# Performance work log

Hardware: AMD Instinct MI355X
Metric: run time of the kernel (lower is better)

Reference implementation:

```python
import jax, jax.numpy as jnp
import numpy as np

SIGMA = 0.05
N_IN, N_OUT, N_HID = 128, 128, 1024
BATCH, LENGTH = 128, 256


def setup_inputs() -> dict:
    key = jax.random.key(0)
    ks = jax.random.split(key, 8)
    input_signal = jax.random.normal(ks[0], (BATCH, LENGTH, N_IN), dtype=jnp.float32)
    hidden = jnp.zeros((BATCH, N_HID), dtype=jnp.float32)
    # learned params (torch nn.Linear stores weight as [out, in])
    W_in = jax.random.normal(ks[1], (N_HID, N_IN), dtype=jnp.float32) / np.sqrt(N_IN)
    W_hh = jax.random.normal(ks[2], (N_HID, N_HID), dtype=jnp.float32) / np.sqrt(N_HID)
    b_hh = jax.random.normal(ks[3], (N_HID,), dtype=jnp.float32) * 0.01
    W_out = jax.random.normal(ks[4], (N_OUT, N_HID), dtype=jnp.float32) / np.sqrt(N_HID)
    # frozen alpha vector (positive, used as sqrt(2/alpha))
    alpha_w = jax.random.uniform(ks[5], (N_HID,), dtype=jnp.float32, minval=5.0, maxval=25.0)
    # per-step noise, shared across batch (torch.randn(n_hid) each step)
    noise = jax.random.normal(ks[6], (LENGTH, N_HID), dtype=jnp.float32)
    return {"input_signal": input_signal, "hidden": hidden, "W_in": W_in,
            "W_hh": W_hh, "b_hh": b_hh, "W_out": W_out,
            "alpha_w": alpha_w, "noise": noise}


def reference(input_signal, hidden, W_in, W_hh, b_hh, W_out, alpha_w, noise):
    # input_signal: [B, T, n_in]; hidden: [B, n_hid]
    x_tbd = jnp.transpose(input_signal, (1, 0, 2))  # [T, B, n_in]
    noise_scale = jnp.sqrt(2.0 / alpha_w) * SIGMA    # [n_hid]

    def step(h, xs):
        x_t, n_t = xs
        pre = x_t @ W_in.T + h @ W_hh.T + b_hh + n_t * noise_scale
        h_new = jax.nn.relu(pre)
        y = h_new @ W_out.T
        return h_new, (h_new, y)

    h_final, (hs, ys) = jax.lax.scan(step, hidden, (x_tbd, noise))
    hidden_list = jnp.transpose(hs, (1, 0, 2))  # [B, T, n_hid]
    output_list = jnp.transpose(ys, (1, 0, 2))  # [B, T, n_out]
    return hidden_list, output_list, h_final
```

## Files before the change

kernel.cpp:

```cpp
#include <hip/hip_runtime.h>
#include <hip/hip_fp16.h>
#include <math.h>


typedef _Float16 half8 __attribute__((ext_vector_type(8)));
typedef float    f32x4 __attribute__((ext_vector_type(4)));
typedef unsigned short ushort8 __attribute__((ext_vector_type(8)));
typedef unsigned int u32x4 __attribute__((ext_vector_type(4)));
typedef unsigned long long u64;

#define SIGMA_F 0.05f

constexpr int T_  = 256;
constexpr int B_  = 128;
constexpr int NH  = 1024;
constexpr int NIN = 128;
constexpr int MB  = 16;

constexpr size_t OFF_XT  = 0;
constexpr size_t OFF_NB  = (size_t)T_*B_*NIN*2;
constexpr size_t OFF_WO  = OFF_NB + (size_t)T_*NH*4;
constexpr size_t OFF_HB  = OFF_WO + (size_t)NIN*NH*2;

__device__ __forceinline__ unsigned short f16bits(float v) {
    return __half_as_ushort(__float2half(v));
}
__device__ __forceinline__ u64 ald(const u64* p) {
    return __hip_atomic_load(p, __ATOMIC_RELAXED, __HIP_MEMORY_SCOPE_AGENT);
}
__device__ __forceinline__ void ast(unsigned int* p, unsigned int v) {
    __hip_atomic_store(p, v, __ATOMIC_RELAXED, __HIP_MEMORY_SCOPE_AGENT);
}

__device__ __forceinline__ void ld8_sc0(u32x4 r[8], const u64* p) {
    asm volatile(
        "global_load_dwordx4 %0, %8, off sc0\n\t"
        "global_load_dwordx4 %1, %8, off offset:256 sc0\n\t"
        "global_load_dwordx4 %2, %8, off offset:512 sc0\n\t"
        "global_load_dwordx4 %3, %8, off offset:768 sc0\n\t"
        "global_load_dwordx4 %4, %8, off offset:1024 sc0\n\t"
        "global_load_dwordx4 %5, %8, off offset:1280 sc0\n\t"
        "global_load_dwordx4 %6, %8, off offset:1536 sc0\n\t"
        "global_load_dwordx4 %7, %8, off offset:1792 sc0\n\t"
        "s_waitcnt vmcnt(0)"
        : "=&v"(r[0]), "=&v"(r[1]), "=&v"(r[2]), "=&v"(r[3]),
          "=&v"(r[4]), "=&v"(r[5]), "=&v"(r[6]), "=&v"(r[7])
        : "v"(p)
        : "memory");
}

__global__ void setup_kernel(const float* __restrict__ X,
                             const float* __restrict__ hidden,
                             const float* __restrict__ b_hh,
                             const float* __restrict__ W_out,
                             const float* __restrict__ alpha_w,
                             const float* __restrict__ noise,
                             unsigned short* __restrict__ Xt,
                             float* __restrict__ NB,
                             unsigned short* __restrict__ Wo,
                             unsigned int* __restrict__ Hb0,
                             unsigned int* __restrict__ Hb1)
{
    int idx = blockIdx.x * 256 + threadIdx.x;
    if (idx < B_ * T_ * NIN) {
        int d = idx & 127, rest = idx >> 7;
        int brow = rest & 127, t = rest >> 7;
        Xt[idx] = f16bits(X[((size_t)brow * T_ + t) * NIN + d]);
    }
    if (idx < T_ * NH) {
        int c = idx & (NH - 1);
        NB[idx] = b_hh[c] + noise[idx] * (sqrtf(2.0f / alpha_w[c]) * SIGMA_F);
    }
    if (idx < NIN * NH) Wo[idx] = f16bits(W_out[idx]);
    if (idx < B_ * NH / 2) {
        unsigned int lo = f16bits(hidden[idx * 2]);
        unsigned int hi = f16bits(hidden[idx * 2 + 1]);
        Hb0[idx] = (lo | (hi << 16)) & 0x7FFF7FFFu;
        Hb1[idx] = 0x80008000u;
    }
}

__global__ __launch_bounds__(256, 1) void rnn_step_kernel(
    const float* __restrict__ W_hh, const float* __restrict__ W_in,
    const unsigned short* __restrict__ Xt, const float* __restrict__ NB,
    unsigned int* __restrict__ Hb0, unsigned int* __restrict__ Hb1,
    float* __restrict__ hidden_list, float* __restrict__ h_final)
{
    __shared__ unsigned short wtile[64 * 960];
    __shared__ unsigned short htile[16 * 1024];

    const int tid = threadIdx.x;
    const int m = blockIdx.x & 7;
    const int n = blockIdx.x >> 3;

    for (int g = tid; g < 64 * 120; g += 256) {
        int row = g / 120, G = g - row * 120;
        const float* s = W_hh + (size_t)(n * 64 + row) * NH + G * 8;
        half8 h;
        #pragma unroll
        for (int j = 0; j < 8; ++j) h[j] = (_Float16)s[j];
        *(half8*)&wtile[row * 960 + ((G ^ (row & 7)) << 3)] = h;
    }

    const int wave = tid >> 6, lane = tid & 63;
    const int l15 = lane & 15, lk = lane >> 4;
    const int colW = wave * 16 + l15;
    const int gcol = n * 64 + colW;

    auto cvt8 = [](const float* s) {
        half8 h;
        #pragma unroll
        for (int j = 0; j < 8; ++j) h[j] = (_Float16)s[j];
        return h;
    };
    half8 bh30 = cvt8(W_hh + (size_t)gcol * NH + 960 + lk * 8);
    half8 bh31 = cvt8(W_hh + (size_t)gcol * NH + 992 + lk * 8);
    half8 bx[4];
    #pragma unroll
    for (int kx = 0; kx < 4; ++kx)
        bx[kx] = cvt8(W_in + (size_t)gcol * NIN + kx * 32 + lk * 8);
    __syncthreads();

    const int hrow = tid >> 4;
    const int part = tid & 15;

    auto xpart = [&](int t) -> f32x4 {
        f32x4 a = {0.f, 0.f, 0.f, 0.f};
        const int rowA = m * MB + l15;
        const ushort8* xp = (const ushort8*)(Xt + ((size_t)t * B_ + rowA) * NIN) + lk;
        #pragma unroll
        for (int kx = 0; kx < 4; ++kx) {
            half8 av = __builtin_bit_cast(half8, xp[kx * 4]);
            a = __builtin_amdgcn_mfma_f32_16x16x32_f16(av, bx[kx], a, 0, 0, 0);
        }
        return a;
    };

    f32x4 accx = xpart(0);

    for (int t = 0; t < T_; ++t) {
        const u64* hp = (const u64*)((t & 1) ? Hb1 : Hb0)
                        + (size_t)(m * MB + hrow) * 256 + part * 2;
        const unsigned int e32 = ((t >> 1) & 1) ? 0x80008000u : 0u;

        u32x4 r[8];
        int round = 0;
        for (;;) {
            if (round < 3) {
                ld8_sc0(r, hp);
            } else {
                #pragma unroll
                for (int j = 0; j < 8; ++j) {
                    u64 a = ald(hp + (size_t)j * 32);
                    u64 b = ald(hp + (size_t)j * 32 + 1);
                    r[j][0] = (unsigned int)a; r[j][1] = (unsigned int)(a >> 32);
                    r[j][2] = (unsigned int)b; r[j][3] = (unsigned int)(b >> 32);
                }
            }
            unsigned int red = 0;
            #pragma unroll
            for (int j = 0; j < 8; ++j) {
                #pragma unroll
                for (int k = 0; k < 4; ++k) red |= r[j][k] ^ e32;
            }
            if (!(red & 0x80008000u)) break;
            ++round;
            if (round >= 3) __builtin_amdgcn_s_sleep(1);
        }

        __syncthreads();

        #pragma unroll
        for (int j = 0; j < 8; ++j) {
            u32x4 w;
            #pragma unroll
            for (int k = 0; k < 4; ++k) w[k] = r[j][k] & 0x7FFF7FFFu;
            int G = j * 16 + part;
            *(half8*)&htile[hrow * 1024 + ((G ^ (hrow & 7)) << 3)] =
                __builtin_bit_cast(half8, w);
        }

        __syncthreads();

        f32x4 acc = accx;
        #pragma unroll
        for (int ki = 0; ki < 30; ++ki) {
            int G = 4 * ki + lk;
            half8 av = *(const half8*)&htile[l15 * 1024 + ((G ^ (l15 & 7)) << 3)];
            half8 bv = *(const half8*)&wtile[colW * 960 + ((G ^ (colW & 7)) << 3)];
            acc = __builtin_amdgcn_mfma_f32_16x16x32_f16(av, bv, acc, 0, 0, 0);
        }
        {
            int G = 120 + lk;
            half8 av = *(const half8*)&htile[l15 * 1024 + ((G ^ (l15 & 7)) << 3)];
            acc = __builtin_amdgcn_mfma_f32_16x16x32_f16(av, bh30, acc, 0, 0, 0);
            G = 124 + lk;
            av = *(const half8*)&htile[l15 * 1024 + ((G ^ (l15 & 7)) << 3)];
            acc = __builtin_amdgcn_mfma_f32_16x16x32_f16(av, bh31, acc, 0, 0, 0);
        }

        const float nb = NB[t * NH + gcol];
        float hv[4];
        #pragma unroll
        for (int r2 = 0; r2 < 4; ++r2) {
            float v = acc[r2] + nb;
            hv[r2] = v > 0.f ? v : 0.f;
        }

        if (t < T_ - 1) {
            unsigned int* hn = (t & 1) ? Hb0 : Hb1;
            const unsigned int tagb = (((t + 1) >> 1) & 1) ? 0x80008000u : 0u;
            #pragma unroll
            for (int r2 = 0; r2 < 4; ++r2) {
                float other = __shfl_xor(hv[r2], 1);
                if (!(lane & 1)) {
                    unsigned int val = (unsigned int)f16bits(hv[r2]) |
                                       ((unsigned int)f16bits(other) << 16) | tagb;
                    int brow = m * MB + lk * 4 + r2;
                    ast(&hn[(size_t)brow * 512 + (gcol >> 1)], val);
                }
            }
        }

        #pragma unroll
        for (int r2 = 0; r2 < 4; ++r2) {
            int brow = m * MB + lk * 4 + r2;
            hidden_list[((size_t)brow * T_ + t) * NH + gcol] = hv[r2];
        }
        if (t == T_ - 1) {
            #pragma unroll
            for (int r2 = 0; r2 < 4; ++r2) {
                int brow = m * MB + lk * 4 + r2;
                h_final[(size_t)brow * NH + gcol] = hv[r2];
            }
        } else {
            accx = xpart(t + 1);
        }
    }
}

__global__ __launch_bounds__(256, 4) void ygemm_kernel(
    const float* __restrict__ HL, const unsigned short* __restrict__ Wo,
    float* __restrict__ Y)
{
    const int tid = threadIdx.x;
    const int wave = tid >> 6, lane = tid & 63;
    const int l15 = lane & 15, lk = lane >> 4;
    const size_t rowbase = (size_t)blockIdx.x * 64;

    f32x4 acc[4][2] = {};

    #pragma unroll 2
    for (int ki = 0; ki < 32; ++ki) {
        const int k0 = ki * 32 + lk * 8;
        half8 bfr[2];
        #pragma unroll
        for (int nt = 0; nt < 2; ++nt) {
            int ncol = (wave * 2 + nt) * 16 + l15;
            ushort8 braw = *(const ushort8*)(Wo + ncol * NH + k0);
            bfr[nt] = __builtin_bit_cast(half8, braw);
        }
        #pragma unroll
        for (int mt = 0; mt < 4; ++mt) {
            size_t row = rowbase + mt * 16 + l15;
            const float4* ap = (const float4*)(HL + row * NH + k0);
            float4 a0 = ap[0];
            float4 a1 = ap[1];
            half8 a = { (_Float16)a0.x, (_Float16)a0.y, (_Float16)a0.z, (_Float16)a0.w,
                        (_Float16)a1.x, (_Float16)a1.y, (_Float16)a1.z, (_Float16)a1.w };
            #pragma unroll
            for (int nt = 0; nt < 2; ++nt)
                acc[mt][nt] = __builtin_amdgcn_mfma_f32_16x16x32_f16(a, bfr[nt], acc[mt][nt], 0, 0, 0);
        }
    }

    #pragma unroll
    for (int mt = 0; mt < 4; ++mt) {
        #pragma unroll
        for (int nt = 0; nt < 2; ++nt) {
            int ncol = (wave * 2 + nt) * 16 + l15;
            #pragma unroll
            for (int r = 0; r < 4; ++r) {
                size_t row = rowbase + mt * 16 + lk * 4 + r;
                Y[row * NIN + ncol] = acc[mt][nt][r];
            }
        }
    }
}

extern "C" void kernel_launch(void* const* d_in, const int* in_sizes, int n_in,
                              void* d_out, int out_size, void* d_ws, size_t ws_size,
                              hipStream_t stream)
{
    const float* X      = (const float*)d_in[0];
    const float* hidden = (const float*)d_in[1];
    const float* W_in   = (const float*)d_in[2];
    const float* W_hh   = (const float*)d_in[3];
    const float* b_hh   = (const float*)d_in[4];
    const float* W_out  = (const float*)d_in[5];
    const float* alpha  = (const float*)d_in[6];
    const float* noise  = (const float*)d_in[7];

    char* ws = (char*)d_ws;
    unsigned short* Xt = (unsigned short*)(ws + OFF_XT);
    float*          NB = (float*)(ws + OFF_NB);
    unsigned short* Wo = (unsigned short*)(ws + OFF_WO);
    unsigned int*  Hb0 = (unsigned int*)(ws + OFF_HB);
    unsigned int*  Hb1 = Hb0 + (size_t)B_ * NH / 2;

    float* hidden_list = (float*)d_out;
    float* output_list = hidden_list + (size_t)B_ * T_ * NH;
    float* h_final     = output_list + (size_t)B_ * T_ * NIN;

    setup_kernel<<<(B_ * T_ * NIN + 255) / 256, 256, 0, stream>>>(
        X, hidden, b_hh, W_out, alpha, noise, Xt, NB, Wo, Hb0, Hb1);

    rnn_step_kernel<<<128, 256, 0, stream>>>(
        W_hh, W_in, Xt, NB, Hb0, Hb1, hidden_list, h_final);

    ygemm_kernel<<<(B_ * T_) / 64, 256, 0, stream>>>(
        hidden_list, Wo, output_list);
}
```

Baseline: 823.2 us.

## Split recurrent GEMM across 256 blocks with intra-block K-split reduction

Each block now owns 32 hidden columns instead of 64, so the grid doubles to 256 blocks. Within a block, the four waves split the K dimension in halves and combine partial sums through a small shared tile. The whole W_hh slice now fits in LDS, so the register-held tail weights go away. This shortens the serial per-step MFMA chain but adds one more barrier per step and doubles the number of blocks in the cross-block spin-wait. Stores of hidden_list become nontemporal and the sc0 polling rounds are raised before the fallback.

```diff
diff --git a/kernel.cpp b/kernel.cpp
--- a/kernel.cpp
+++ b/kernel.cpp
@@ -5,7 +5,6 @@
 
 typedef _Float16 half8 __attribute__((ext_vector_type(8)));
 typedef float    f32x4 __attribute__((ext_vector_type(4)));
-typedef unsigned short ushort8 __attribute__((ext_vector_type(8)));
 typedef unsigned int u32x4 __attribute__((ext_vector_type(4)));
 typedef unsigned long long u64;
 
@@ -16,6 +15,7 @@
 constexpr int NH  = 1024;
 constexpr int NIN = 128;
 constexpr int MB  = 16;
+constexpr int NCB = 32;
 
 constexpr size_t OFF_XT  = 0;
 constexpr size_t OFF_NB  = (size_t)T_*B_*NIN*2;
@@ -86,26 +86,29 @@
     unsigned int* __restrict__ Hb0, unsigned int* __restrict__ Hb1,
     float* __restrict__ hidden_list, float* __restrict__ h_final)
 {
-    __shared__ unsigned short wtile[64 * 960];
+    __shared__ unsigned short wtile[NCB * 1024];
     __shared__ unsigned short htile[16 * 1024];
+    __shared__ f32x4 rtile[2][64];
 
     const int tid = threadIdx.x;
     const int m = blockIdx.x & 7;
     const int n = blockIdx.x >> 3;
 
-    for (int g = tid; g < 64 * 120; g += 256) {
-        int row = g / 120, G = g - row * 120;
-        const float* s = W_hh + (size_t)(n * 64 + row) * NH + G * 8;
+    for (int g = tid; g < NCB * 128; g += 256) {
+        int row = g >> 7, G = g & 127;
+        const float* s = W_hh + (size_t)(n * NCB + row) * NH + G * 8;
         half8 h;
         #pragma unroll
         for (int j = 0; j < 8; ++j) h[j] = (_Float16)s[j];
-        *(half8*)&wtile[row * 960 + ((G ^ (row & 7)) << 3)] = h;
+        *(half8*)&wtile[row * 1024 + ((G ^ (row & 7)) << 3)] = h;
     }
 
     const int wave = tid >> 6, lane = tid & 63;
+    const int c  = wave & 1;
+    const int kh = wave >> 1;
     const int l15 = lane & 15, lk = lane >> 4;
-    const int colW = wave * 16 + l15;
-    const int gcol = n * 64 + colW;
+    const int colW = c * 16 + l15;
+    const int gcol = n * NCB + colW;
 
     auto cvt8 = [](const float* s) {
         half8 h;
@@ -113,26 +116,24 @@
         for (int j = 0; j < 8; ++j) h[j] = (_Float16)s[j];
         return h;
     };
-    half8 bh30 = cvt8(W_hh + (size_t)gcol * NH + 960 + lk * 8);
-    half8 bh31 = cvt8(W_hh + (size_t)gcol * NH + 992 + lk * 8);
-    half8 bx[4];
+    half8 bx2[2];
     #pragma unroll
-    for (int kx = 0; kx < 4; ++kx)
-        bx[kx] = cvt8(W_in + (size_t)gcol * NIN + kx * 32 + lk * 8);
+    for (int j = 0; j < 2; ++j)
+        bx2[j] = cvt8(W_in + (size_t)gcol * NIN + (2 * kh + j) * 32 + lk * 8);
     __syncthreads();
 
     const int hrow = tid >> 4;
     const int part = tid & 15;
 
+    const int rowA = m * MB + l15;
+
     auto xpart = [&](int t) -> f32x4 {
         f32x4 a = {0.f, 0.f, 0.f, 0.f};
-        const int rowA = m * MB + l15;
-        const ushort8* xp = (const ushort8*)(Xt + ((size_t)t * B_ + rowA) * NIN) + lk;
-        #pragma unroll
-        for (int kx = 0; kx < 4; ++kx) {
-            half8 av = __builtin_bit_cast(half8, xp[kx * 4]);
-            a = __builtin_amdgcn_mfma_f32_16x16x32_f16(av, bx[kx], a, 0, 0, 0);
-        }
+        const half8* xp = (const half8*)(Xt + ((size_t)t * B_ + rowA) * NIN);
+        #pragma unroll
+        for (int j = 0; j < 2; ++j)
+            a = __builtin_amdgcn_mfma_f32_16x16x32_f16(
+                    xp[(2 * kh + j) * 4 + lk], bx2[j], a, 0, 0, 0);
         return a;
     };
 
@@ -144,28 +145,30 @@
         const unsigned int e32 = ((t >> 1) & 1) ? 0x80008000u : 0u;
 
         u32x4 r[8];
-        int round = 0;
-        for (;;) {
-            if (round < 3) {
-                ld8_sc0(r, hp);
-            } else {
+        {
+            int round = 0;
+            for (;;) {
+                if (round < 6) {
+                    ld8_sc0(r, hp);
+                } else {
+                    #pragma unroll
+                    for (int j = 0; j < 8; ++j) {
+                        u64 a = ald(hp + (size_t)j * 32);
+                        u64 b = ald(hp + (size_t)j * 32 + 1);
+                        r[j][0] = (unsigned int)a; r[j][1] = (unsigned int)(a >> 32);
+                        r[j][2] = (unsigned int)b; r[j][3] = (unsigned int)(b >> 32);
+                    }
+                }
+                unsigned int red = 0;
                 #pragma unroll
                 for (int j = 0; j < 8; ++j) {
-                    u64 a = ald(hp + (size_t)j * 32);
-                    u64 b = ald(hp + (size_t)j * 32 + 1);
-                    r[j][0] = (unsigned int)a; r[j][1] = (unsigned int)(a >> 32);
-                    r[j][2] = (unsigned int)b; r[j][3] = (unsigned int)(b >> 32);
+                    #pragma unroll
+                    for (int k = 0; k < 4; ++k) red |= r[j][k] ^ e32;
                 }
-            }
-            unsigned int red = 0;
-            #pragma unroll
-            for (int j = 0; j < 8; ++j) {
-                #pragma unroll
-                for (int k = 0; k < 4; ++k) red |= r[j][k] ^ e32;
-            }
-            if (!(red & 0x80008000u)) break;
-            ++round;
-            if (round >= 3) __builtin_amdgcn_s_sleep(1);
+                if (!(red & 0x80008000u)) break;
+                ++round;
+                if (round >= 3) __builtin_amdgcn_s_sleep(1);
+            }
         }
 
         __syncthreads();
@@ -184,58 +187,58 @@
 
         f32x4 acc = accx;
         #pragma unroll
-        for (int ki = 0; ki < 30; ++ki) {
+        for (int ki0 = 0; ki0 < 16; ++ki0) {
+            int ki = 16 * kh + ki0;
             int G = 4 * ki + lk;
             half8 av = *(const half8*)&htile[l15 * 1024 + ((G ^ (l15 & 7)) << 3)];
-            half8 bv = *(const half8*)&wtile[colW * 960 + ((G ^ (colW & 7)) << 3)];
+            half8 bv = *(const half8*)&wtile[colW * 1024 + ((G ^ (colW & 7)) << 3)];
             acc = __builtin_amdgcn_mfma_f32_16x16x32_f16(av, bv, acc, 0, 0, 0);
         }
-        {
-            int G = 120 + lk;
-            half8 av = *(const half8*)&htile[l15 * 1024 + ((G ^ (l15 & 7)) << 3)];
-            acc = __builtin_amdgcn_mfma_f32_16x16x32_f16(av, bh30, acc, 0, 0, 0);
-            G = 124 + lk;
-            av = *(const half8*)&htile[l15 * 1024 + ((G ^ (l15 & 7)) << 3)];
-            acc = __builtin_amdgcn_mfma_f32_16x16x32_f16(av, bh31, acc, 0, 0, 0);
-        }
-
-        const float nb = NB[t * NH + gcol];
-        float hv[4];
-        #pragma unroll
-        for (int r2 = 0; r2 < 4; ++r2) {
-            float v = acc[r2] + nb;
-            hv[r2] = v > 0.f ? v : 0.f;
-        }
-
-        if (t < T_ - 1) {
-            unsigned int* hn = (t & 1) ? Hb0 : Hb1;
-            const unsigned int tagb = (((t + 1) >> 1) & 1) ? 0x80008000u : 0u;
+
+        if (kh == 1) rtile[c][lane] = acc;
+        __syncthreads();
+
+        if (kh == 0) {
+            f32x4 o = rtile[c][lane];
+            const float nb = NB[t * NH + gcol];
+            float hv[4];
             #pragma unroll
             for (int r2 = 0; r2 < 4; ++r2) {
-                float other = __shfl_xor(hv[r2], 1);
-                if (!(lane & 1)) {
-                    unsigned int val = (unsigned int)f16bits(hv[r2]) |
-                                       ((unsigned int)f16bits(other) << 16) | tagb;
-                    int brow = m * MB + lk * 4 + r2;
-                    ast(&hn[(size_t)brow * 512 + (gcol >> 1)], val);
+                float v = acc[r2] + o[r2] + nb;
+                hv[r2] = v > 0.f ? v : 0.f;
+            }
+
+            if (t < T_ - 1) {
+                unsigned int* hn = (t & 1) ? Hb0 : Hb1;
+                const unsigned int tagb = (((t + 1) >> 1) & 1) ? 0x80008000u : 0u;
+                #pragma unroll
+                for (int r2 = 0; r2 < 4; ++r2) {
+                    float other = __shfl_xor(hv[r2], 1);
+                    if (!(lane & 1)) {
+                        unsigned int val = (unsigned int)f16bits(hv[r2]) |
+                                           ((unsigned int)f16bits(other) << 16) | tagb;
+                        int brow = m * MB + lk * 4 + r2;
+                        ast(&hn[(size_t)brow * 512 + (gcol >> 1)], val);
+                    }
                 }
             }
-        }
-
-        #pragma unroll
-        for (int r2 = 0; r2 < 4; ++r2) {
-            int brow = m * MB + lk * 4 + r2;
-            hidden_list[((size_t)brow * T_ + t) * NH + gcol] = hv[r2];
-        }
-        if (t == T_ - 1) {
+
             #pragma unroll
             for (int r2 = 0; r2 < 4; ++r2) {
                 int brow = m * MB + lk * 4 + r2;
-                h_final[(size_t)brow * NH + gcol] = hv[r2];
-            }
-        } else {
-            accx = xpart(t + 1);
-        }
+                __builtin_nontemporal_store(
+                    hv[r2], &hidden_list[((size_t)brow * T_ + t) * NH + gcol]);
+            }
+            if (t == T_ - 1) {
+                #pragma unroll
+                for (int r2 = 0; r2 < 4; ++r2) {
+                    int brow = m * MB + lk * 4 + r2;
+                    __builtin_nontemporal_store(
+                        hv[r2], &h_final[(size_t)brow * NH + gcol]);
+                }
+            }
+        }
+        if (t < T_ - 1) accx = xpart(t + 1);
     }
 }
 
@@ -243,6 +246,7 @@
     const float* __restrict__ HL, const unsigned short* __restrict__ Wo,
     float* __restrict__ Y)
 {
+    typedef unsigned short ushort8 __attribute__((ext_vector_type(8)));
     const int tid = threadIdx.x;
     const int wave = tid >> 6, lane = tid & 63;
     const int l15 = lane & 15, lk = lane >> 4;
@@ -315,7 +319,7 @@
     setup_kernel<<<(B_ * T_ * NIN + 255) / 256, 256, 0, stream>>>(
         X, hidden, b_hh, W_out, alpha, noise, Xt, NB, Wo, Hb0, Hb1);
 
-    rnn_step_kernel<<<128, 256, 0, stream>>>(
+    rnn_step_kernel<<<256, 256, 0, stream>>>(
         W_hh, W_in, Xt, NB, Hb0, Hb1, hidden_list, h_final);
 
     ygemm_kernel<<<(B_ * T_) / 64, 256, 0, stream>>>(
```

Result: slower. 1.766 ms (+114.5%).

## Add per-step per-row-group ready flags before polling tagged hidden state

Applied to the files above, without the earlier changes.

Adds a flag array with one flag per (timestep, batch group, producer wave). Each producer wave sets its flag after its hidden-state stores drain, and consumers poll a single dword per lane until all 64 flags are set before reading the tagged hidden buffers. The intent is to replace repeated polling of large 8x16B hidden loads with a cheap flag poll. The cost is an extra vmcnt wait plus a flag store on the producer side, and extra latency on the critical step-to-step path, while the old tag-check loop is still kept as a fallback.

```diff
diff --git a/kernel.cpp b/kernel.cpp
--- a/kernel.cpp
+++ b/kernel.cpp
@@ -5,7 +5,6 @@
 
 typedef _Float16 half8 __attribute__((ext_vector_type(8)));
 typedef float    f32x4 __attribute__((ext_vector_type(4)));
-typedef unsigned short ushort8 __attribute__((ext_vector_type(8)));
 typedef unsigned int u32x4 __attribute__((ext_vector_type(4)));
 typedef unsigned long long u64;
 
@@ -21,11 +20,15 @@
 constexpr size_t OFF_NB  = (size_t)T_*B_*NIN*2;
 constexpr size_t OFF_WO  = OFF_NB + (size_t)T_*NH*4;
 constexpr size_t OFF_HB  = OFF_WO + (size_t)NIN*NH*2;
+constexpr size_t OFF_FLG = OFF_HB + (size_t)2*B_*(NH/2)*4;
 
 __device__ __forceinline__ unsigned short f16bits(float v) {
     return __half_as_ushort(__float2half(v));
 }
 __device__ __forceinline__ u64 ald(const u64* p) {
+    return __hip_atomic_load(p, __ATOMIC_RELAXED, __HIP_MEMORY_SCOPE_AGENT);
+}
+__device__ __forceinline__ unsigned int ald32(const unsigned int* p) {
     return __hip_atomic_load(p, __ATOMIC_RELAXED, __HIP_MEMORY_SCOPE_AGENT);
 }
 __device__ __forceinline__ void ast(unsigned int* p, unsigned int v) {
@@ -49,6 +52,15 @@
         : "memory");
 }
 
+__device__ __forceinline__ unsigned int ld_flag_sc0(const unsigned int* p) {
+    unsigned int v;
+    asm volatile(
+        "global_load_dword %0, %1, off sc0\n\t"
+        "s_waitcnt vmcnt(0)"
+        : "=v"(v) : "v"(p) : "memory");
+    return v;
+}
+
 __global__ void setup_kernel(const float* __restrict__ X,
                              const float* __restrict__ hidden,
                              const float* __restrict__ b_hh,
@@ -59,7 +71,8 @@
                              float* __restrict__ NB,
                              unsigned short* __restrict__ Wo,
                              unsigned int* __restrict__ Hb0,
-                             unsigned int* __restrict__ Hb1)
+                             unsigned int* __restrict__ Hb1,
+                             unsigned int* __restrict__ FLG)
 {
     int idx = blockIdx.x * 256 + threadIdx.x;
     if (idx < B_ * T_ * NIN) {
@@ -78,12 +91,14 @@
         Hb0[idx] = (lo | (hi << 16)) & 0x7FFF7FFFu;
         Hb1[idx] = 0x80008000u;
     }
+    if (idx < T_ * 8 * 64) FLG[idx] = (idx < 8 * 64) ? 1u : 0u;
 }
 
 __global__ __launch_bounds__(256, 1) void rnn_step_kernel(
     const float* __restrict__ W_hh, const float* __restrict__ W_in,
     const unsigned short* __restrict__ Xt, const float* __restrict__ NB,
     unsigned int* __restrict__ Hb0, unsigned int* __restrict__ Hb1,
+    unsigned int* __restrict__ FLG,
     float* __restrict__ hidden_list, float* __restrict__ h_final)
 {
     __shared__ unsigned short wtile[64 * 960];
@@ -124,48 +139,60 @@
     const int hrow = tid >> 4;
     const int part = tid & 15;
 
+    const int rowA = m * MB + l15;
+
     auto xpart = [&](int t) -> f32x4 {
         f32x4 a = {0.f, 0.f, 0.f, 0.f};
-        const int rowA = m * MB + l15;
-        const ushort8* xp = (const ushort8*)(Xt + ((size_t)t * B_ + rowA) * NIN) + lk;
-        #pragma unroll
-        for (int kx = 0; kx < 4; ++kx) {
-            half8 av = __builtin_bit_cast(half8, xp[kx * 4]);
-            a = __builtin_amdgcn_mfma_f32_16x16x32_f16(av, bx[kx], a, 0, 0, 0);
-        }
+        const half8* xp = (const half8*)(Xt + ((size_t)t * B_ + rowA) * NIN) + lk;
+        #pragma unroll
+        for (int kx = 0; kx < 4; ++kx)
+            a = __builtin_amdgcn_mfma_f32_16x16x32_f16(xp[kx * 4], bx[kx], a, 0, 0, 0);
         return a;
     };
 
     f32x4 accx = xpart(0);
 
     for (int t = 0; t < T_; ++t) {
+        {
+            const unsigned int* fp = FLG + ((size_t)t * 8 + m) * 64 + lane;
+            int fr = 0;
+            for (;;) {
+                unsigned int fv = (fr < 6) ? ld_flag_sc0(fp) : ald32(fp);
+                if (__all(fv != 0u)) break;
+                ++fr;
+                if (fr >= 2) __builtin_amdgcn_s_sleep(2);
+            }
+        }
+
         const u64* hp = (const u64*)((t & 1) ? Hb1 : Hb0)
                         + (size_t)(m * MB + hrow) * 256 + part * 2;
         const unsigned int e32 = ((t >> 1) & 1) ? 0x80008000u : 0u;
 
         u32x4 r[8];
-        int round = 0;
-        for (;;) {
-            if (round < 3) {
-                ld8_sc0(r, hp);
-            } else {
+        {
+            int round = 0;
+            for (;;) {
+                if (round < 6) {
+                    ld8_sc0(r, hp);
+                } else {
+                    #pragma unroll
+                    for (int j = 0; j < 8; ++j) {
+                        u64 a = ald(hp + (size_t)j * 32);
+                        u64 b = ald(hp + (size_t)j * 32 + 1);
+                        r[j][0] = (unsigned int)a; r[j][1] = (unsigned int)(a >> 32);
+                        r[j][2] = (unsigned int)b; r[j][3] = (unsigned int)(b >> 32);
+                    }
+                }
+                unsigned int red = 0;
                 #pragma unroll
                 for (int j = 0; j < 8; ++j) {
-                    u64 a = ald(hp + (size_t)j * 32);
-                    u64 b = ald(hp + (size_t)j * 32 + 1);
-                    r[j][0] = (unsigned int)a; r[j][1] = (unsigned int)(a >> 32);
-                    r[j][2] = (unsigned int)b; r[j][3] = (unsigned int)(b >> 32);
+                    #pragma unroll
+                    for (int k = 0; k < 4; ++k) red |= r[j][k] ^ e32;
                 }
-            }
-            unsigned int red = 0;
-            #pragma unroll
-            for (int j = 0; j < 8; ++j) {
-                #pragma unroll
-                for (int k = 0; k < 4; ++k) red |= r[j][k] ^ e32;
-            }
-            if (!(red & 0x80008000u)) break;
-            ++round;
-            if (round >= 3) __builtin_amdgcn_s_sleep(1);
+                if (!(red & 0x80008000u)) break;
+                ++round;
+                if (round >= 3) __builtin_amdgcn_s_sleep(1);
+            }
         }
 
         __syncthreads();
@@ -220,6 +247,9 @@
                     ast(&hn[(size_t)brow * 512 + (gcol >> 1)], val);
                 }
             }
+            asm volatile("s_waitcnt vmcnt(0)" ::: "memory");
+            if (lane == 0)
+                ast(FLG + ((size_t)(t + 1) * 8 + m) * 64 + n * 4 + wave, 1u);
         }
 
         #pragma unroll
@@ -243,6 +273,7 @@
     const float* __restrict__ HL, const unsigned short* __restrict__ Wo,
     float* __restrict__ Y)
 {
+    typedef unsigned short ushort8 __attribute__((ext_vector_type(8)));
     const int tid = threadIdx.x;
     const int wave = tid >> 6, lane = tid & 63;
     const int l15 = lane & 15, lk = lane >> 4;
@@ -307,16 +338,17 @@
     unsigned short* Wo = (unsigned short*)(ws + OFF_WO);
     unsigned int*  Hb0 = (unsigned int*)(ws + OFF_HB);
     unsigned int*  Hb1 = Hb0 + (size_t)B_ * NH / 2;
+    unsigned int*  FLG = (unsigned int*)(ws + OFF_FLG);
 
     float* hidden_list = (float*)d_out;
     float* output_list = hidden_list + (size_t)B_ * T_ * NH;
     float* h_final     = output_list + (size_t)B_ * T_ * NIN;
 
     setup_kernel<<<(B_ * T_ * NIN + 255) / 256, 256, 0, stream>>>(
-        X, hidden, b_hh, W_out, alpha, noise, Xt, NB, Wo, Hb0, Hb1);
+        X, hidden, b_hh, W_out, alpha, noise, Xt, NB, Wo, Hb0, Hb1, FLG);
 
     rnn_step_kernel<<<128, 256, 0, stream>>>(
-        W_hh, W_in, Xt, NB, Hb0, Hb1, hidden_list, h_final);
+        W_hh, W_in, Xt, NB, Hb0, Hb1, FLG, hidden_list, h_final);
 
     ygemm_kernel<<<(B_ * T_) / 64, 256, 0, stream>>>(
         hidden_list, Wo, output_list);
```

New measurement: 1.010 ms. 22.7% more time.
